# Kernel optimization log

Measured on AMD Instinct MI355X. Metric: run time of the kernel, lower is better.

## Reference

```python
import jax, jax.numpy as jnp
import numpy as np

OUT, IN, GS = 8192, 8192, 128
N_GROUPS = OUT * IN // GS  # 524288


def setup_inputs() -> dict:
    key = jax.random.key(0)
    k1, k2, k3 = jax.random.split(key, 3)
    x = jax.random.normal(k1, (32, IN), dtype=jnp.float32)
    # ternary values in {-1, 0, 1}
    ternary = jax.random.randint(k2, (OUT, IN), -1, 2, dtype=jnp.int32)
    # positive per-group scales
    scales = jax.random.uniform(k3, (N_GROUPS,), dtype=jnp.float32, minval=0.01, maxval=0.1)
    return {"x": x, "ternary": ternary, "scales": scales}


def reference(x, ternary, scales):
    # Dequantize: each contiguous group of GS weights shares one scale.
    # scales: [n_groups] -> [n_groups, GS] -> [OUT, IN]
    scales_exp = jnp.broadcast_to(scales[:, None], (N_GROUPS, GS)).reshape(OUT, IN)
    w = ternary.astype(jnp.float32) * scales_exp  # [OUT, IN]
    # F.linear(x, w) = x @ w.T
    return jnp.einsum("ti,oi->to", x, w)
```

## Files before the change

### kernel.cpp

```cpp
#include <hip/hip_runtime.h>
#include <stdint.h>

#define OUT_DIM 8192
#define IN_DIM  8192
#define GS      128
#define MROWS   32
#define NSPLIT  8
#define PART_ELEMS (MROWS * OUT_DIM)

typedef __attribute__((ext_vector_type(8))) short bf16x8;
typedef __attribute__((ext_vector_type(4))) float f32x4;
typedef __attribute__((ext_vector_type(8))) unsigned short u16x8;

__device__ __forceinline__ unsigned short f2bf_rne(float f) {
    uint32_t v = __builtin_bit_cast(uint32_t, f);
    v += 0x7FFFu + ((v >> 16) & 1u);
    return (unsigned short)(v >> 16);
}

__device__ __forceinline__ bf16x8 pack8(float4 a, float4 b) {
    u16x8 u;
    u[0] = f2bf_rne(a.x); u[1] = f2bf_rne(a.y);
    u[2] = f2bf_rne(a.z); u[3] = f2bf_rne(a.w);
    u[4] = f2bf_rne(b.x); u[5] = f2bf_rne(b.y);
    u[6] = f2bf_rne(b.z); u[7] = f2bf_rne(b.w);
    return __builtin_bit_cast(bf16x8, u);
}

__global__ __launch_bounds__(256) void ternary_gemm(
    const int* __restrict__ tern, const float* __restrict__ scales,
    const float* __restrict__ x, float* __restrict__ part) {
    const int wave  = blockIdx.x * 4 + (threadIdx.x >> 6);
    const int lane  = threadIdx.x & 63;
    const int kc    = wave >> 9;
    const int ntile = wave & 511;
    const int n     = lane & 15;
    const int quad  = lane >> 4;
    const int o      = (ntile << 4) + n;
    const int k0base = kc << 10;

    const int* __restrict__ wrow = tern + (size_t)o * IN_DIM;
    const float* __restrict__ xr0 = x + n * IN_DIM;
    const float* __restrict__ xr1 = x + (16 + n) * IN_DIM;

    const float* __restrict__ sp = scales + o * (IN_DIM / GS) + (kc << 3);
    float s_cur = sp[0];

    f32x4 acc0 = {0.f, 0.f, 0.f, 0.f};
    f32x4 acc1 = {0.f, 0.f, 0.f, 0.f};

#pragma unroll 1
    for (int it = 0; it < 8; ++it) {
        const unsigned int p = f2bf_rne(s_cur);
        float s_nxt = sp[(it < 7) ? (it + 1) : 7];
        const int k0 = k0base + (it << 7);
#pragma unroll
        for (int st = 0; st < 4; ++st) {
            const int k = k0 + (st << 5) + (quad << 3);
            int4 w0 = *(const int4*)(wrow + k);
            int4 w1 = *(const int4*)(wrow + k + 4);
            float4 xf00 = *(const float4*)(xr0 + k);
            float4 xf01 = *(const float4*)(xr0 + k + 4);
            float4 xf10 = *(const float4*)(xr1 + k);
            float4 xf11 = *(const float4*)(xr1 + k + 4);
            bf16x8 a0 = pack8(xf00, xf01);
            bf16x8 a1 = pack8(xf10, xf11);
            int tw[8] = {w0.x, w0.y, w0.z, w0.w, w1.x, w1.y, w1.z, w1.w};
            bf16x8 bfr;
#pragma unroll
            for (int j = 0; j < 8; ++j) {
                int t = tw[j];
                unsigned int v = p | ((unsigned int)t & 0x8000u);
                bfr[j] = (short)((t == 0) ? 0u : v);
            }
            acc0 = __builtin_amdgcn_mfma_f32_16x16x32_bf16(a0, bfr, acc0, 0, 0, 0);
            acc1 = __builtin_amdgcn_mfma_f32_16x16x32_bf16(a1, bfr, acc1, 0, 0, 0);
        }
        s_cur = s_nxt;
    }

    float* __restrict__ prow = part + (size_t)kc * PART_ELEMS;
#pragma unroll
    for (int r = 0; r < 4; ++r) {
        prow[(quad * 4 + r) * OUT_DIM + o]        = acc0[r];
        prow[(quad * 4 + r + 16) * OUT_DIM + o]   = acc1[r];
    }
}

__global__ __launch_bounds__(256) void reduce_parts(const float* __restrict__ part,
                                                    float* __restrict__ out) {
    const int i = (blockIdx.x * 256 + threadIdx.x) * 4;
    float4 s = *(const float4*)(part + i);
#pragma unroll
    for (int kc = 1; kc < NSPLIT; ++kc) {
        float4 v = *(const float4*)(part + (size_t)kc * PART_ELEMS + i);
        s.x += v.x; s.y += v.y; s.z += v.z; s.w += v.w;
    }
    *(float4*)(out + i) = s;
}

extern "C" void kernel_launch(void* const* d_in, const int* in_sizes, int n_in,
                              void* d_out, int out_size, void* d_ws, size_t ws_size,
                              hipStream_t stream) {
    const float* x      = (const float*)d_in[0];
    const int*   tern   = (const int*)d_in[1];
    const float* scales = (const float*)d_in[2];
    float* out = (float*)d_out;

    float* part = (float*)d_ws;

    ternary_gemm<<<1024, 256, 0, stream>>>(tern, scales, x, part);
    reduce_parts<<<256, 256, 0, stream>>>(part, out);
}
```

Measured before the change: 424.6 us.

## Double the K-split to 16 chunks and software-prefetch ternary weights

The split-K factor goes from 8 to 16, so each wave covers 512 K elements instead of 1024 and the grid doubles to 2048 blocks, giving more waves in flight to hide memory latency on the 256 MB int32 weight stream. The inner loop now loads the next step's weight vectors before issuing the current MFMAs, so global loads overlap with the conversion and matrix work. In exchange, the partial-sum workspace and the reduction work double (16 partial buffers of 32x8192 floats), and the reduce kernel reads more data.

After: 417.7 us. No clear change (-1.6%).

```diff
diff --git a/kernel.cpp b/kernel.cpp
--- a/kernel.cpp
+++ b/kernel.cpp
@@ -5,7 +5,8 @@
 #define IN_DIM  8192
 #define GS      128
 #define MROWS   32
-#define NSPLIT  8
+#define NSPLIT  16
+#define KCHUNK  512
 #define PART_ELEMS (MROWS * OUT_DIM)
 
 typedef __attribute__((ext_vector_type(8))) short bf16x8;
@@ -36,33 +37,37 @@
     const int ntile = wave & 511;
     const int n     = lane & 15;
     const int quad  = lane >> 4;
-    const int o      = (ntile << 4) + n;
-    const int k0base = kc << 10;
+    const int o     = (ntile << 4) + n;
+    const int kbase = (kc << 9) + (quad << 3);
 
-    const int* __restrict__ wrow = tern + (size_t)o * IN_DIM;
-    const float* __restrict__ xr0 = x + n * IN_DIM;
-    const float* __restrict__ xr1 = x + (16 + n) * IN_DIM;
+    const int*   __restrict__ wrow = tern + (size_t)o * IN_DIM + kbase;
+    const float* __restrict__ xr0  = x + n * IN_DIM + kbase;
+    const float* __restrict__ xr1  = x + (16 + n) * IN_DIM + kbase;
 
-    const float* __restrict__ sp = scales + o * (IN_DIM / GS) + (kc << 3);
+    const float* __restrict__ sp = scales + o * (IN_DIM / GS) + (kc << 2);
     float s_cur = sp[0];
 
     f32x4 acc0 = {0.f, 0.f, 0.f, 0.f};
     f32x4 acc1 = {0.f, 0.f, 0.f, 0.f};
 
+    int4 w0 = *(const int4*)(wrow + 0);
+    int4 w1 = *(const int4*)(wrow + 4);
+
 #pragma unroll 1
-    for (int it = 0; it < 8; ++it) {
+    for (int g = 0; g < 4; ++g) {
         const unsigned int p = f2bf_rne(s_cur);
-        float s_nxt = sp[(it < 7) ? (it + 1) : 7];
-        const int k0 = k0base + (it << 7);
+        float s_nxt = sp[(g < 3) ? (g + 1) : 3];
 #pragma unroll
         for (int st = 0; st < 4; ++st) {
-            const int k = k0 + (st << 5) + (quad << 3);
-            int4 w0 = *(const int4*)(wrow + k);
-            int4 w1 = *(const int4*)(wrow + k + 4);
-            float4 xf00 = *(const float4*)(xr0 + k);
-            float4 xf01 = *(const float4*)(xr0 + k + 4);
-            float4 xf10 = *(const float4*)(xr1 + k);
-            float4 xf11 = *(const float4*)(xr1 + k + 4);
+            const int koff  = (g << 7) + (st << 5);
+            const int knext = (st < 3) ? (koff + 32)
+                                       : ((g < 3) ? ((g + 1) << 7) : koff);
+            int4 nw0 = *(const int4*)(wrow + knext);
+            int4 nw1 = *(const int4*)(wrow + knext + 4);
+            float4 xf00 = *(const float4*)(xr0 + koff);
+            float4 xf01 = *(const float4*)(xr0 + koff + 4);
+            float4 xf10 = *(const float4*)(xr1 + koff);
+            float4 xf11 = *(const float4*)(xr1 + koff + 4);
             bf16x8 a0 = pack8(xf00, xf01);
             bf16x8 a1 = pack8(xf10, xf11);
             int tw[8] = {w0.x, w0.y, w0.z, w0.w, w1.x, w1.y, w1.z, w1.w};
@@ -75,6 +80,7 @@
             }
             acc0 = __builtin_amdgcn_mfma_f32_16x16x32_bf16(a0, bfr, acc0, 0, 0, 0);
             acc1 = __builtin_amdgcn_mfma_f32_16x16x32_bf16(a1, bfr, acc1, 0, 0, 0);
+            w0 = nw0; w1 = nw1;
         }
         s_cur = s_nxt;
     }
@@ -109,6 +115,6 @@
 
     float* part = (float*)d_ws;
 
-    ternary_gemm<<<1024, 256, 0, stream>>>(tern, scales, x, part);
+    ternary_gemm<<<NSPLIT * 512 / 4, 256, 0, stream>>>(tern, scales, x, part);
     reduce_parts<<<256, 256, 0, stream>>>(part, out);
 }
```
